# Kernel optimization log

Measured on AMD Instinct MI355X. Metric: run time of the kernel, lower is better.

Reference implementation:

```python
import jax, jax.numpy as jnp
import numpy as np

B, Q, KV, D, H = 2, 2048, 2048, 1024, 16
DH = D // H  # 64


def _rmsnorm(x, w, eps):
    return x * jax.lax.rsqrt(jnp.mean(x * x, axis=-1, keepdims=True) + eps) * w


def setup_inputs() -> dict:
    k0 = jax.random.key(0)
    ks = jax.random.split(k0, 7)
    s = 0.02
    return {
        "query": jax.random.normal(ks[0], (B, Q, D), jnp.float32),
        "key": jax.random.normal(ks[1], (B, KV, D), jnp.float32),
        "value": jax.random.normal(ks[2], (B, KV, D), jnp.float32),
        # RMSNorm weights (init to ones like nn.RMSNorm)
        "wq_norm": jnp.ones((D,), jnp.float32),
        "wk_norm": jnp.ones((D,), jnp.float32),
        # MHA in-projection for q and k (Wv / out_proj never affect attn weights)
        "Wq": jax.random.normal(ks[3], (D, D), jnp.float32) * s,
        "Wk": jax.random.normal(ks[4], (D, D), jnp.float32) * s,
        "bq": jax.random.normal(ks[5], (D,), jnp.float32) * s,
        "bk": jax.random.normal(ks[6], (D,), jnp.float32) * s,
    }


def reference(query, key, value, wq_norm, wk_norm, Wq, Wk, bq, bk):
    eps = jnp.finfo(query.dtype).eps  # nn.RMSNorm default eps
    qn = _rmsnorm(query, wq_norm, eps)
    kn = _rmsnorm(key, wk_norm, eps)
    # MHA in-projections (torch Linear: x @ W.T + b), split into heads
    q = (qn @ Wq.T + bq).reshape(B, Q, H, DH)
    k = (kn @ Wk.T + bk).reshape(B, KV, H, DH)
    # per-head scaled dot-product scores [B,H,Q,KV]
    scores = jnp.einsum('bihd,bjhd->bhij', q, k) / np.float32(np.sqrt(DH))
    # softmax over keys, then average over heads (average_attn_weights=True)
    attn = jax.nn.softmax(scores, axis=-1).mean(axis=1)  # [B,Q,KV]
    # custom re-weighting of the *separate* value tensor
    features = jnp.einsum('bij,bjd->bid', attn, value)  # [B,Q,D]
    return features
```

## Files before the change

kernel.cpp:

```cpp
#include <hip/hip_runtime.h>

#define B_  2
#define Q_  2048
#define KV_ 2048
#define D_  1024
#define H_  16
#define DH_ 64

#define QSCALE 0.18033688011112042f

using u16 = unsigned short;
using bf16x8 = __attribute__((ext_vector_type(8))) short;
using f32x4  = __attribute__((ext_vector_type(4))) float;

__device__ __forceinline__ u16 f2bf(float x) {
  unsigned u = __float_as_uint(x);
  u += 0x7fffu + ((u >> 16) & 1u);
  return (u16)(u >> 16);
}

__device__ __forceinline__ void gl_lds16(const void* g, void* l) {
  __builtin_amdgcn_global_load_lds(
      (const __attribute__((address_space(1))) void*)g,
      (__attribute__((address_space(3))) void*)l, 16, 0, 0);
}

template<int N> __device__ __forceinline__ void wait_vmcnt() {
  if constexpr (N == 0)      asm volatile("s_waitcnt vmcnt(0)" ::: "memory");
  else if constexpr (N == 2) asm volatile("s_waitcnt vmcnt(2)" ::: "memory");
  else if constexpr (N == 3) asm volatile("s_waitcnt vmcnt(3)" ::: "memory");
  else if constexpr (N == 4) asm volatile("s_waitcnt vmcnt(4)" ::: "memory");
  else if constexpr (N == 6) asm volatile("s_waitcnt vmcnt(6)" ::: "memory");
  else if constexpr (N == 8) asm volatile("s_waitcnt vmcnt(8)" ::: "memory");
}
__device__ __forceinline__ void barrier_raw() {
  asm volatile("" ::: "memory");
  __builtin_amdgcn_s_barrier();
  asm volatile("" ::: "memory");
}

#define MFMA16(a, b, c) __builtin_amdgcn_mfma_f32_16x16x32_bf16((a), (b), (c), 0, 0, 0)
#define EXP2F(x) __builtin_amdgcn_exp2f(x)

__global__ __launch_bounds__(256) void k_prep(
    const float* __restrict__ q, const float* __restrict__ k,
    const float* __restrict__ wq, const float* __restrict__ wk,
    const float* __restrict__ Wq, const float* __restrict__ Wk,
    const float* __restrict__ bq, const float* __restrict__ bk,
    const float* __restrict__ v,
    u16* __restrict__ qn, u16* __restrict__ kn,
    u16* __restrict__ Wb, float* __restrict__ biasbuf,
    u16* __restrict__ vT)
{
  __shared__ char smem[64 * 72 * 2];
  const int bid = blockIdx.x, t = threadIdx.x;
  if (bid < 2048) {
    const int w = t >> 6, lane = t & 63;
    const int row = bid * 4 + w;
    const float* src; const float* wgt; u16* dst;
    if (row < B_ * Q_) {
      src = q + (size_t)row * D_; wgt = wq; dst = qn + (size_t)row * D_;
    } else {
      const int r2 = row - B_ * Q_;
      src = k + (size_t)r2 * D_; wgt = wk; dst = kn + (size_t)r2 * D_;
    }
    float4 v4[4];
    float ss = 0.f;
    #pragma unroll
    for (int i = 0; i < 4; ++i) {
      v4[i] = reinterpret_cast<const float4*>(src)[lane + 64 * i];
      ss += v4[i].x * v4[i].x + v4[i].y * v4[i].y
          + v4[i].z * v4[i].z + v4[i].w * v4[i].w;
    }
    #pragma unroll
    for (int off = 1; off < 64; off <<= 1) ss += __shfl_xor(ss, off);
    const float sc = rsqrtf(ss * (1.0f / D_) + 1.1920929e-07f);
    #pragma unroll
    for (int i = 0; i < 4; ++i) {
      const float4 wv = reinterpret_cast<const float4*>(wgt)[lane + 64 * i];
      ushort4 o;
      o.x = f2bf(v4[i].x * sc * wv.x);
      o.y = f2bf(v4[i].y * sc * wv.y);
      o.z = f2bf(v4[i].z * sc * wv.z);
      o.w = f2bf(v4[i].w * sc * wv.w);
      reinterpret_cast<ushort4*>(dst)[lane + 64 * i] = o;
    }
  } else if (bid < 3072) {
    const int pb = bid - 2048;
    #pragma unroll
    for (int rr = 0; rr < 2; ++rr) {
      const int i = pb * 512 + rr * 256 + t;
      const bool isK = i >= 262144;
      const int j = i & 262143;
      float4 vv = reinterpret_cast<const float4*>(isK ? Wk : Wq)[j];
      ushort4 o;
      o.x = f2bf(vv.x); o.y = f2bf(vv.y); o.z = f2bf(vv.z); o.w = f2bf(vv.w);
      reinterpret_cast<ushort4*>(Wb + (isK ? D_ * D_ : 0))[j] = o;
    }
  } else if (bid == 3072) {
    #pragma unroll
    for (int rr = 0; rr < 2; ++rr) {
      const int i = rr * 256 + t;
      float4 vv = (i < 256) ? reinterpret_cast<const float4*>(bq)[i]
                            : reinterpret_cast<const float4*>(bk)[i - 256];
      reinterpret_cast<float4*>(biasbuf)[i] = vv;
    }
  } else {
    const int tb = bid - 3073;
    const int kv0 = (tb & 31) * 64, d0 = ((tb >> 5) & 15) * 64, b = tb >> 9;
    u16 (*tile)[72] = (u16(*)[72])smem;
    #pragma unroll
    for (int i = 0; i < 16; ++i) {
      const int idx = i * 256 + t, r = idx >> 6, c = idx & 63;
      tile[r][c] = f2bf(v[((size_t)b * KV_ + kv0 + r) * D_ + d0 + c]);
    }
    __syncthreads();
    #pragma unroll
    for (int i = 0; i < 16; ++i) {
      const int idx = i * 256 + t, r = idx >> 6, c = idx & 63;
      vT[((size_t)b * D_ + d0 + r) * KV_ + kv0 + c] = tile[c][r];
    }
  }
}

template<int TM, int TN, int WM, int WN, bool OUT_BF16, bool PROJ>
__global__ __launch_bounds__(512) void k_gemm_bt(
    const u16* __restrict__ A, int lda, long sA,
    const u16* __restrict__ Bm, int ldb, long sB,
    void* __restrict__ C, int ldc, long sC,
    int K, const float* __restrict__ bias)
{
  constexpr int RM = TM / WM / 16, RN = TN / WN / 16;
  constexpr int LA = TM / 64, LB = TN / 64;
  constexpr int NL = LA + LB;
  const int bb = blockIdx.z;
  const u16* Ab = A + (size_t)bb * sA;
  const u16* Bb = Bm + (size_t)bb * sB;
  const int row0 = blockIdx.y * TM, col0 = blockIdx.x * TN;
  __shared__ u16 As[2][TM * 64];
  __shared__ u16 Bs[2][TN * 64];
  const int tid = threadIdx.x, lane = tid & 63;
  const int w = tid >> 6, wm = w / WN, wn = w % WN;
  const int lrow = lane & 15, sub = lane >> 4, lrow7 = lrow & 7;
  const f32x4 zero4 = {0.f, 0.f, 0.f, 0.f};
  f32x4 acc[RM][RN];
  #pragma unroll
  for (int m = 0; m < RM; ++m)
    #pragma unroll
    for (int n = 0; n < RN; ++n) acc[m][n] = zero4;

  const int nk = K >> 6;

#define GEMM_STAGE(buf, kt)                                                   \
  {                                                                           \
    const int k0 = (kt) << 6;                                                 \
    _Pragma("unroll")                                                         \
    for (int i = 0; i < LA; ++i) {                                            \
      const int c = i * 512 + tid, r = c >> 3, u = (c & 7) ^ (r & 7);         \
      gl_lds16(Ab + (size_t)(row0 + r) * lda + k0 + u * 8, &As[buf][c * 8]);  \
    }                                                                         \
    _Pragma("unroll")                                                         \
    for (int i = 0; i < LB; ++i) {                                            \
      const int c = i * 512 + tid, r = c >> 3, u = (c & 7) ^ (r & 7);         \
      gl_lds16(Bb + (size_t)(col0 + r) * ldb + k0 + u * 8, &Bs[buf][c * 8]);  \
    }                                                                         \
  }

  GEMM_STAGE(0, 0);
  int cur = 0;
  for (int kt = 0; kt < nk; ++kt) {
    if (kt + 1 < nk) {
      GEMM_STAGE(cur ^ 1, kt + 1);
      wait_vmcnt<NL>();
    } else {
      wait_vmcnt<0>();
    }
    barrier_raw();
    #pragma unroll
    for (int ks = 0; ks < 2; ++ks) {
      bf16x8 af[RM], bfr[RN];
      #pragma unroll
      for (int m = 0; m < RM; ++m) {
        const int rA = wm * (TM / WM) + m * 16 + lrow;
        af[m] = *(const bf16x8*)&As[cur][rA * 64 + ((((ks << 2) + sub) ^ lrow7) << 3)];
      }
      #pragma unroll
      for (int n = 0; n < RN; ++n) {
        const int rB = wn * (TN / WN) + n * 16 + lrow;
        bfr[n] = *(const bf16x8*)&Bs[cur][rB * 64 + ((((ks << 2) + sub) ^ lrow7) << 3)];
      }
      #pragma unroll
      for (int m = 0; m < RM; ++m)
        #pragma unroll
        for (int n = 0; n < RN; ++n)
          acc[m][n] = MFMA16(af[m], bfr[n], acc[m][n]);
    }
    barrier_raw();
    cur ^= 1;
  }
#undef GEMM_STAGE

  const int crow = sub * 4, ccol = lane & 15;
  const float scl = (PROJ && bb == 0) ? QSCALE : 1.0f;
  #pragma unroll
  for (int m = 0; m < RM; ++m) {
    #pragma unroll
    for (int n = 0; n < RN; ++n) {
      const int gcol = col0 + wn * (TN / WN) + n * 16 + ccol;
      const float badd = PROJ ? bias[bb * 1024 + gcol] : 0.0f;
      #pragma unroll
      for (int r = 0; r < 4; ++r) {
        const int grow = row0 + wm * (TM / WM) + m * 16 + crow + r;
        const float val = (acc[m][n][r] + badd) * scl;
        if (OUT_BF16)
          ((u16*)C)[(size_t)bb * sC + (size_t)grow * ldc + gcol] = f2bf(val);
        else
          ((float*)C)[(size_t)bb * sC + (size_t)grow * ldc + gcol] = val;
      }
    }
  }
}

__global__ __launch_bounds__(512) void k_attn_rowsum(
    const u16* __restrict__ qp, const u16* __restrict__ kp,
    float* __restrict__ Linv)
{
  const int qb = blockIdx.x * 128, h = blockIdx.y, b = blockIdx.z;
  __shared__ u16 Aq[128 * 64];
  __shared__ u16 Kk[2][128 * 64];
  __shared__ float red[4][128];
  const int tid = threadIdx.x, lane = tid & 63, w = tid >> 6;
  const int wm = w >> 2, wn = w & 3;
  const int lrow = lane & 15, sub = lane >> 4, lrow7 = lrow & 7;

  #pragma unroll
  for (int i = 0; i < 2; ++i) {
    const int c = i * 512 + tid, r = c >> 3, u = (c & 7) ^ (r & 7);
    gl_lds16(&qp[((size_t)b * Q_ + qb + r) * D_ + h * 64 + u * 8], &Aq[c * 8]);
  }

#define STAGE_KK(buf, kvt)                                                    \
  {                                                                           \
    _Pragma("unroll")                                                         \
    for (int i = 0; i < 2; ++i) {                                             \
      const int c = i * 512 + tid, r = c >> 3, u = (c & 7) ^ (r & 7);         \
      gl_lds16(&kp[((size_t)b * KV_ + (kvt) * 128 + r) * D_ + h * 64 + u * 8],\
               &Kk[buf][c * 8]);                                              \
    }                                                                         \
  }

  STAGE_KK(0, 0);
  const f32x4 zero4 = {0.f, 0.f, 0.f, 0.f};
  float lsum[4][4];
  #pragma unroll
  for (int m = 0; m < 4; ++m)
    #pragma unroll
    for (int r = 0; r < 4; ++r) lsum[m][r] = 0.f;
  bf16x8 af[4][2];

  for (int kvt = 0; kvt < KV_ / 128; ++kvt) {
    const int cur = kvt & 1;
    if (kvt + 1 < KV_ / 128) {
      STAGE_KK(cur ^ 1, kvt + 1);
      wait_vmcnt<2>();
    } else {
      wait_vmcnt<0>();
    }
    barrier_raw();
    if (kvt == 0) {
      #pragma unroll
      for (int m = 0; m < 4; ++m) {
        const int rA = wm * 64 + m * 16 + lrow;
        af[m][0] = *(const bf16x8*)&Aq[rA * 64 + ((sub ^ lrow7) << 3)];
        af[m][1] = *(const bf16x8*)&Aq[rA * 64 + (((4 + sub) ^ lrow7) << 3)];
      }
    }
    bf16x8 bf[2][2];
    #pragma unroll
    for (int n = 0; n < 2; ++n) {
      const int rB = wn * 32 + n * 16 + lrow;
      bf[n][0] = *(const bf16x8*)&Kk[cur][rB * 64 + ((sub ^ lrow7) << 3)];
      bf[n][1] = *(const bf16x8*)&Kk[cur][rB * 64 + (((4 + sub) ^ lrow7) << 3)];
    }
    __builtin_amdgcn_s_setprio(1);
    #pragma unroll
    for (int m = 0; m < 4; ++m) {
      #pragma unroll
      for (int n = 0; n < 2; ++n) {
        f32x4 s = zero4;
        s = MFMA16(af[m][0], bf[n][0], s);
        s = MFMA16(af[m][1], bf[n][1], s);
        #pragma unroll
        for (int r = 0; r < 4; ++r) lsum[m][r] += EXP2F(s[r]);
      }
    }
    __builtin_amdgcn_s_setprio(0);
    barrier_raw();
  }
#undef STAGE_KK

  #pragma unroll
  for (int m = 0; m < 4; ++m)
    #pragma unroll
    for (int r = 0; r < 4; ++r) {
      #pragma unroll
      for (int off = 1; off < 16; off <<= 1)
        lsum[m][r] += __shfl_xor(lsum[m][r], off);
    }
  if (lrow == 0) {
    #pragma unroll
    for (int m = 0; m < 4; ++m)
      #pragma unroll
      for (int r = 0; r < 4; ++r)
        red[wn][wm * 64 + m * 16 + sub * 4 + r] = lsum[m][r];
  }
  __syncthreads();
  if (tid < 128) {
    const float s = red[0][tid] + red[1][tid] + red[2][tid] + red[3][tid];
    Linv[((size_t)b * H_ + h) * Q_ + qb + tid] = 1.0f / (s * (float)H_);
  }
}

__global__ __launch_bounds__(512) void k_attn_weights(
    const u16* __restrict__ qp, const u16* __restrict__ kp,
    const float* __restrict__ Linv, u16* __restrict__ attn)
{
  const int kv0 = blockIdx.x * 128, qb = blockIdx.y * 128, b = blockIdx.z;
  __shared__ u16 As[2][128 * 64];
  __shared__ u16 Bs[2][128 * 64];
  __shared__ float linv_s[H_][128];
  const int tid = threadIdx.x, lane = tid & 63, w = tid >> 6;
  const int wm = w >> 2, wn = w & 3;
  const int lrow = lane & 15, sub = lane >> 4, lrow7 = lrow & 7;

  {
    const int hh = tid >> 5, i0 = (tid & 31) * 4;
    *reinterpret_cast<float4*>(&linv_s[hh][i0]) =
        *reinterpret_cast<const float4*>(&Linv[((size_t)b * H_ + hh) * Q_ + qb + i0]);
  }
  __syncthreads();

#define STAGE_AB(buf, hh)                                                     \
  {                                                                           \
    _Pragma("unroll")                                                         \
    for (int i = 0; i < 2; ++i) {                                             \
      const int c = i * 512 + tid, r = c >> 3, u = (c & 7) ^ (r & 7);         \
      gl_lds16(&qp[((size_t)b * Q_ + qb + r) * D_ + (hh) * 64 + u * 8],       \
               &As[buf][c * 8]);                                              \
      gl_lds16(&kp[((size_t)b * KV_ + kv0 + r) * D_ + (hh) * 64 + u * 8],     \
               &Bs[buf][c * 8]);                                              \
    }                                                                         \
  }

  const f32x4 zero4 = {0.f, 0.f, 0.f, 0.f};
  f32x4 acc[4][2];
  #pragma unroll
  for (int m = 0; m < 4; ++m)
    #pragma unroll
    for (int n = 0; n < 2; ++n) acc[m][n] = zero4;

  STAGE_AB(0, 0);
  for (int h = 0; h < H_; ++h) {
    const int cur = h & 1;
    if (h + 1 < H_) {
      STAGE_AB(cur ^ 1, h + 1);
      wait_vmcnt<4>();
    } else {
      wait_vmcnt<0>();
    }
    barrier_raw();
    bf16x8 af[4][2], bf[2][2];
    #pragma unroll
    for (int m = 0; m < 4; ++m) {
      const int rA = wm * 64 + m * 16 + lrow;
      af[m][0] = *(const bf16x8*)&As[cur][rA * 64 + ((sub ^ lrow7) << 3)];
      af[m][1] = *(const bf16x8*)&As[cur][rA * 64 + (((4 + sub) ^ lrow7) << 3)];
    }
    #pragma unroll
    for (int n = 0; n < 2; ++n) {
      const int rB = wn * 32 + n * 16 + lrow;
      bf[n][0] = *(const bf16x8*)&Bs[cur][rB * 64 + ((sub ^ lrow7) << 3)];
      bf[n][1] = *(const bf16x8*)&Bs[cur][rB * 64 + (((4 + sub) ^ lrow7) << 3)];
    }
    f32x4 lv[4];
    #pragma unroll
    for (int m = 0; m < 4; ++m)
      lv[m] = *(const f32x4*)&linv_s[h][wm * 64 + m * 16 + sub * 4];
    __builtin_amdgcn_s_setprio(1);
    #pragma unroll
    for (int m = 0; m < 4; ++m) {
      #pragma unroll
      for (int n = 0; n < 2; ++n) {
        f32x4 s = zero4;
        s = MFMA16(af[m][0], bf[n][0], s);
        s = MFMA16(af[m][1], bf[n][1], s);
        #pragma unroll
        for (int r = 0; r < 4; ++r)
          acc[m][n][r] += EXP2F(s[r]) * lv[m][r];
      }
    }
    __builtin_amdgcn_s_setprio(0);
    barrier_raw();
  }
#undef STAGE_AB

  #pragma unroll
  for (int m = 0; m < 4; ++m) {
    #pragma unroll
    for (int n = 0; n < 2; ++n) {
      const int gcol = kv0 + wn * 32 + n * 16 + lrow;
      #pragma unroll
      for (int r = 0; r < 4; ++r) {
        const int grow = qb + wm * 64 + m * 16 + sub * 4 + r;
        attn[((size_t)b * Q_ + grow) * KV_ + gcol] = f2bf(acc[m][n][r]);
      }
    }
  }
}

extern "C" void kernel_launch(void* const* d_in, const int* in_sizes, int n_in,
                              void* d_out, int out_size, void* d_ws, size_t ws_size,
                              hipStream_t stream)
{
  (void)in_sizes; (void)n_in; (void)out_size; (void)ws_size;
  const float* query = (const float*)d_in[0];
  const float* key   = (const float*)d_in[1];
  const float* value = (const float*)d_in[2];
  const float* wqn   = (const float*)d_in[3];
  const float* wkn   = (const float*)d_in[4];
  const float* Wq    = (const float*)d_in[5];
  const float* Wk    = (const float*)d_in[6];
  const float* bq    = (const float*)d_in[7];
  const float* bk    = (const float*)d_in[8];
  float* out = (float*)d_out;

  char* ws = (char*)d_ws;
  u16* qn   = (u16*)(ws);
  u16* attn = (u16*)(ws);
  u16* qp   = (u16*)(ws + 16777216);
  u16* kp   = (u16*)(ws + 25165824);
  u16* Wqb  = (u16*)(ws + 33554432);
  u16* vT   = (u16*)(ws + 37748736);
  float* Linv = (float*)(ws + 46137344);
  float* biasbuf = (float*)(ws + 46399488);
  u16* kn = qn + 4194304;

  k_prep<<<dim3(4097), dim3(256), 0, stream>>>(
      query, key, wqn, wkn, Wq, Wk, bq, bk, value, qn, kn, Wqb, biasbuf, vT);

  k_gemm_bt<128, 128, 2, 4, true, true>
      <<<dim3(D_ / 128, (B_ * Q_) / 128, 2), dim3(512), 0, stream>>>(
      qn, D_, 4194304, Wqb, D_, 1048576, qp, D_, 4194304, D_, biasbuf);

  k_attn_rowsum<<<dim3(Q_ / 128, H_, B_), dim3(512), 0, stream>>>(qp, kp, Linv);
  k_attn_weights<<<dim3(KV_ / 128, Q_ / 128, B_), dim3(512), 0, stream>>>(qp, kp, Linv, attn);

  k_gemm_bt<128, 64, 4, 2, false, false>
      <<<dim3(D_ / 64, Q_ / 128, B_), dim3(512), 0, stream>>>(
      attn, KV_, (long)Q_ * KV_, vT, KV_, (long)D_ * KV_,
      out, D_, (long)Q_ * D_, KV_, nullptr);
}
```

Baseline: 126.4 us.

## Add dedicated 256x128 triple-buffered projection GEMM with split MFMA phases

```diff
diff --git a/kernel.cpp b/kernel.cpp
--- a/kernel.cpp
+++ b/kernel.cpp
@@ -26,7 +26,10 @@
 }
 
 template<int N> __device__ __forceinline__ void wait_vmcnt() {
+  static_assert(N == 0 || N == 1 || N == 2 || N == 3 || N == 4 ||
+                N == 6 || N == 8, "wait_vmcnt: unsupported N");
   if constexpr (N == 0)      asm volatile("s_waitcnt vmcnt(0)" ::: "memory");
+  else if constexpr (N == 1) asm volatile("s_waitcnt vmcnt(1)" ::: "memory");
   else if constexpr (N == 2) asm volatile("s_waitcnt vmcnt(2)" ::: "memory");
   else if constexpr (N == 3) asm volatile("s_waitcnt vmcnt(3)" ::: "memory");
   else if constexpr (N == 4) asm volatile("s_waitcnt vmcnt(4)" ::: "memory");
@@ -123,12 +126,120 @@
   }
 }
 
-template<int TM, int TN, int WM, int WN, bool OUT_BF16, bool PROJ>
+__global__ __launch_bounds__(512) void k_gemm_proj8(
+    const u16* __restrict__ A, long sA,
+    const u16* __restrict__ Bm, long sB,
+    u16* __restrict__ C, long sC,
+    const float* __restrict__ bias)
+{
+  const int bb = blockIdx.z;
+  const u16* Ab = A + (size_t)bb * sA;
+  const u16* Bb = Bm + (size_t)bb * sB;
+  const int row0 = blockIdx.y * 256, col0 = blockIdx.x * 128;
+  __shared__ u16 As3[3][256 * 64];
+  __shared__ u16 Bs3[3][128 * 64];
+  const int tid = threadIdx.x, lane = tid & 63;
+  const int w = tid >> 6, wm = w >> 1, wn = w & 1;
+  const int lrow = lane & 15, sub = lane >> 4, lrow7 = lrow & 7;
+  const f32x4 zero4 = {0.f, 0.f, 0.f, 0.f};
+  f32x4 acc[4][4];
+  #pragma unroll
+  for (int m = 0; m < 4; ++m)
+    #pragma unroll
+    for (int n = 0; n < 4; ++n) acc[m][n] = zero4;
+
+  const int nk = D_ >> 6;
+
+#define PSTAGE(buf, kt)                                                       \
+  {                                                                           \
+    const int k0 = (kt) << 6;                                                 \
+    _Pragma("unroll")                                                         \
+    for (int i = 0; i < 4; ++i) {                                             \
+      const int c = i * 512 + tid, r = c >> 3, u = (c & 7) ^ (r & 7);         \
+      gl_lds16(Ab + (size_t)(row0 + r) * D_ + k0 + u * 8, &As3[buf][c * 8]);  \
+    }                                                                         \
+    _Pragma("unroll")                                                         \
+    for (int i = 0; i < 2; ++i) {                                             \
+      const int c = i * 512 + tid, r = c >> 3, u = (c & 7) ^ (r & 7);         \
+      gl_lds16(Bb + (size_t)(col0 + r) * D_ + k0 + u * 8, &Bs3[buf][c * 8]);  \
+    }                                                                         \
+  }
+
+  PSTAGE(0, 0);
+  PSTAGE(1, 1);
+  for (int t = 0; t < nk; ++t) {
+    const int cb = t % 3;
+    if (t + 1 < nk) wait_vmcnt<6>();
+    else            wait_vmcnt<0>();
+    barrier_raw();
+    bf16x8 af[4][2], bf0[2][2];
+    #pragma unroll
+    for (int m = 0; m < 4; ++m) {
+      const int rA = wm * 64 + m * 16 + lrow;
+      af[m][0] = *(const bf16x8*)&As3[cb][rA * 64 + ((sub ^ lrow7) << 3)];
+      af[m][1] = *(const bf16x8*)&As3[cb][rA * 64 + (((4 + sub) ^ lrow7) << 3)];
+    }
+    #pragma unroll
+    for (int n = 0; n < 2; ++n) {
+      const int rB = wn * 64 + n * 16 + lrow;
+      bf0[n][0] = *(const bf16x8*)&Bs3[cb][rB * 64 + ((sub ^ lrow7) << 3)];
+      bf0[n][1] = *(const bf16x8*)&Bs3[cb][rB * 64 + (((4 + sub) ^ lrow7) << 3)];
+    }
+    if (t + 2 < nk) PSTAGE((t + 2) % 3, t + 2);
+    barrier_raw();
+    __builtin_amdgcn_s_setprio(1);
+    #pragma unroll
+    for (int m = 0; m < 4; ++m)
+      #pragma unroll
+      for (int n = 0; n < 2; ++n) {
+        acc[m][n] = MFMA16(af[m][0], bf0[n][0], acc[m][n]);
+        acc[m][n] = MFMA16(af[m][1], bf0[n][1], acc[m][n]);
+      }
+    __builtin_amdgcn_s_setprio(0);
+    barrier_raw();
+    bf16x8 bf1[2][2];
+    #pragma unroll
+    for (int n = 0; n < 2; ++n) {
+      const int rB = wn * 64 + (n + 2) * 16 + lrow;
+      bf1[n][0] = *(const bf16x8*)&Bs3[cb][rB * 64 + ((sub ^ lrow7) << 3)];
+      bf1[n][1] = *(const bf16x8*)&Bs3[cb][rB * 64 + (((4 + sub) ^ lrow7) << 3)];
+    }
+    barrier_raw();
+    __builtin_amdgcn_s_setprio(1);
+    #pragma unroll
+    for (int m = 0; m < 4; ++m)
+      #pragma unroll
+      for (int n = 0; n < 2; ++n) {
+        acc[m][n + 2] = MFMA16(af[m][0], bf1[n][0], acc[m][n + 2]);
+        acc[m][n + 2] = MFMA16(af[m][1], bf1[n][1], acc[m][n + 2]);
+      }
+    __builtin_amdgcn_s_setprio(0);
+  }
+#undef PSTAGE
+
+  const int crow = sub * 4, ccol = lane & 15;
+  const float scl = (bb == 0) ? QSCALE : 1.0f;
+  #pragma unroll
+  for (int m = 0; m < 4; ++m) {
+    #pragma unroll
+    for (int n = 0; n < 4; ++n) {
+      const int gcol = col0 + wn * 64 + n * 16 + ccol;
+      const float badd = bias[bb * 1024 + gcol];
+      #pragma unroll
+      for (int r = 0; r < 4; ++r) {
+        const int grow = row0 + wm * 64 + m * 16 + crow + r;
+        C[(size_t)bb * sC + (size_t)grow * D_ + gcol] =
+            f2bf((acc[m][n][r] + badd) * scl);
+      }
+    }
+  }
+}
+
+template<int TM, int TN, int WM, int WN, bool OUT_BF16>
 __global__ __launch_bounds__(512) void k_gemm_bt(
     const u16* __restrict__ A, int lda, long sA,
     const u16* __restrict__ Bm, int ldb, long sB,
-    void* __restrict__ C, int ldc, long sC,
-    int K, const float* __restrict__ bias)
+    void* __restrict__ C, int ldc, long sC, int K)
 {
   constexpr int RM = TM / WM / 16, RN = TN / WN / 16;
   constexpr int LA = TM / 64, LB = TN / 64;
@@ -201,17 +312,15 @@
 #undef GEMM_STAGE
 
   const int crow = sub * 4, ccol = lane & 15;
-  const float scl = (PROJ && bb == 0) ? QSCALE : 1.0f;
   #pragma unroll
   for (int m = 0; m < RM; ++m) {
     #pragma unroll
     for (int n = 0; n < RN; ++n) {
       const int gcol = col0 + wn * (TN / WN) + n * 16 + ccol;
-      const float badd = PROJ ? bias[bb * 1024 + gcol] : 0.0f;
       #pragma unroll
       for (int r = 0; r < 4; ++r) {
         const int grow = row0 + wm * (TM / WM) + m * 16 + crow + r;
-        const float val = (acc[m][n][r] + badd) * scl;
+        const float val = acc[m][n][r];
         if (OUT_BF16)
           ((u16*)C)[(size_t)bb * sC + (size_t)grow * ldc + gcol] = f2bf(val);
         else
@@ -448,15 +557,14 @@
   k_prep<<<dim3(4097), dim3(256), 0, stream>>>(
       query, key, wqn, wkn, Wq, Wk, bq, bk, value, qn, kn, Wqb, biasbuf, vT);
 
-  k_gemm_bt<128, 128, 2, 4, true, true>
-      <<<dim3(D_ / 128, (B_ * Q_) / 128, 2), dim3(512), 0, stream>>>(
-      qn, D_, 4194304, Wqb, D_, 1048576, qp, D_, 4194304, D_, biasbuf);
+  k_gemm_proj8<<<dim3(D_ / 128, (B_ * Q_) / 256, 2), dim3(512), 0, stream>>>(
+      qn, 4194304, Wqb, 1048576, qp, 4194304, biasbuf);
 
   k_attn_rowsum<<<dim3(Q_ / 128, H_, B_), dim3(512), 0, stream>>>(qp, kp, Linv);
   k_attn_weights<<<dim3(KV_ / 128, Q_ / 128, B_), dim3(512), 0, stream>>>(qp, kp, Linv, attn);
 
-  k_gemm_bt<128, 64, 4, 2, false, false>
+  k_gemm_bt<128, 64, 4, 2, false>
       <<<dim3(D_ / 64, Q_ / 128, B_), dim3(512), 0, stream>>>(
       attn, KV_, (long)Q_ * KV_, vT, KV_, (long)D_ * KV_,
-      out, D_, (long)Q_ * D_, KV_, nullptr);
-}
+      out, D_, (long)Q_ * D_, KV_);
+}
```

Measured after the change: 130.1 us. 1.03x slower.
